# Optimization experiments

Measured on AMD Instinct MI355X. Metric: run time of the kernel, lower is better.

Reference implementation:

```python
import jax, jax.numpy as jnp
import numpy as np

B, S, D = 2, 2048, 2048
H, KVH, DH = 16, 4, 128  # n_heads, n_kv_heads, head_dim
N_REP = H // KVH
THETA = 10000.0


def setup_inputs() -> dict:
    key = jax.random.key(0)
    ks = jax.random.split(key, 6)
    x = jax.random.normal(ks[0], (B, S, D), dtype=jnp.float32)
    wq = jax.random.normal(ks[1], (H * DH, D), dtype=jnp.float32) * (D ** -0.5)
    wk = jax.random.normal(ks[2], (KVH * DH, D), dtype=jnp.float32) * (D ** -0.5)
    wv = jax.random.normal(ks[3], (KVH * DH, D), dtype=jnp.float32) * (D ** -0.5)
    wo = jax.random.normal(ks[4], (D, H * DH), dtype=jnp.float32) * (D ** -0.5)
    # RoPE frequencies (complex freqs -> cos/sin), shape [S, DH//2]
    inv_freq = 1.0 / (THETA ** (np.arange(0, DH, 2, dtype=np.float32) / DH))
    angles = np.arange(S, dtype=np.float32)[:, None] * inv_freq[None, :]
    freqs_cos = jnp.asarray(np.cos(angles))
    freqs_sin = jnp.asarray(np.sin(angles))
    # causal additive mask [1,1,S,S]
    neg = jnp.full((S, S), -1e9, dtype=jnp.float32)
    mask = jnp.triu(neg, k=1)[None, None]
    return {"x": x, "freqs_cos": freqs_cos, "freqs_sin": freqs_sin,
            "mask": mask, "wq": wq, "wk": wk, "wv": wv, "wo": wo}


def _rope(t, cos, sin):
    # t: [B,S,h,DH]; cos/sin: [S,DH//2] -> broadcast [1,S,1,DH//2]
    tp = t.reshape(*t.shape[:-1], -1, 2)
    tr, ti = tp[..., 0], tp[..., 1]
    c = cos[None, :, None, :]
    s = sin[None, :, None, :]
    out_r = tr * c - ti * s
    out_i = tr * s + ti * c
    return jnp.stack([out_r, out_i], axis=-1).reshape(t.shape)


def reference(x, freqs_cos, freqs_sin, mask, wq, wk, wv, wo):
    b, s, _ = x.shape
    xq = jnp.einsum('bsd,ed->bse', x, wq).reshape(b, s, H, DH)
    xk = jnp.einsum('bsd,ed->bse', x, wk).reshape(b, s, KVH, DH)
    xv = jnp.einsum('bsd,ed->bse', x, wv).reshape(b, s, KVH, DH)
    xq = _rope(xq, freqs_cos, freqs_sin)
    xk = _rope(xk, freqs_cos, freqs_sin)
    # GQA: repeat kv heads
    xk = jnp.repeat(xk, N_REP, axis=2)
    xv = jnp.repeat(xv, N_REP, axis=2)
    q = xq.transpose(0, 2, 1, 3)  # [B,H,S,DH]
    k = xk.transpose(0, 2, 1, 3)
    v = xv.transpose(0, 2, 1, 3)
    scores = jnp.einsum('bhqd,bhkd->bhqk', q, k) / jnp.sqrt(jnp.float32(DH))
    scores = scores + mask
    attn = jax.nn.softmax(scores.astype(jnp.float32), axis=-1).astype(q.dtype)
    out = jnp.einsum('bhqk,bhkd->bhqd', attn, v)
    out = out.transpose(0, 2, 1, 3).reshape(b, s, H * DH)
    return jnp.einsum('bse,de->bsd', out, wo)
```

## Files before the change

kernel.cpp:

```cpp
#include <hip/hip_runtime.h>

#define Bq   2
#define Sq   2048
#define Dq   2048
#define Hq   16
#define KVHq 4
#define DHq  128

typedef unsigned short u16;
typedef short  bf16x8 __attribute__((ext_vector_type(8)));
typedef float  f32x4  __attribute__((ext_vector_type(4)));
typedef float  f32x16 __attribute__((ext_vector_type(16)));
typedef unsigned short u16x2 __attribute__((ext_vector_type(2)));
typedef unsigned short u16x4 __attribute__((ext_vector_type(4)));
typedef unsigned uu32x4 __attribute__((ext_vector_type(4)));

__device__ __forceinline__ u16 f2bf(float f) {
    unsigned u = __float_as_uint(f);
    u += 0x7fffu + ((u >> 16) & 1u);
    return (u16)(u >> 16);
}
__device__ __forceinline__ float bf2f(u16 s) {
    return __uint_as_float(((unsigned)s) << 16);
}

__device__ __forceinline__ unsigned cvtpk(float a, float b) {
    unsigned r;
    asm("v_cvt_pk_bf16_f32 %0, %1, %2" : "=v"(r) : "v"(a), "v"(b));
    return r;
}
__device__ __forceinline__ void pl32swap(unsigned& a, unsigned& b) {
    asm("v_permlane32_swap_b32 %0, %1" : "+v"(a), "+v"(b));
}
__device__ __forceinline__ bf16x8 mkfrag(unsigned w0, unsigned w1, unsigned w2, unsigned w3) {
    uu32x4 t = {w0, w1, w2, w3};
    return __builtin_bit_cast(bf16x8, t);
}

__global__ void cast_all(const float* __restrict__ x,
                         const float* __restrict__ wq, const float* __restrict__ wk,
                         const float* __restrict__ wv, const float* __restrict__ wo,
                         u16* __restrict__ xb, u16* __restrict__ wqb,
                         u16* __restrict__ wkvb, u16* __restrict__ wob) {
    int i = blockIdx.x * 256 + threadIdx.x;
    const float4* src; u16x4* dst; int off;
    if (i < 2097152) { src = (const float4*)x; dst = (u16x4*)xb; off = i; }
    else {
        int j = i - 2097152;
        if (j < 1048576)      { src = (const float4*)wq; dst = (u16x4*)wqb;  off = j; }
        else if (j < 1310720) { src = (const float4*)wk; dst = (u16x4*)wkvb; off = j - 1048576; }
        else if (j < 1572864) { src = (const float4*)wv; dst = (u16x4*)wkvb + 262144; off = j - 1310720; }
        else                  { src = (const float4*)wo; dst = (u16x4*)wob;  off = j - 1572864; }
    }
    float4 v = src[off];
    u16x4 o;
    o.x = f2bf(v.x); o.y = f2bf(v.y); o.z = f2bf(v.z); o.w = f2bf(v.w);
    dst[off] = o;
}

__device__ __forceinline__ void async16(const void* g, void* l) {
    __builtin_amdgcn_global_load_lds(
        (const __attribute__((address_space(1))) unsigned*)g,
        (__attribute__((address_space(3))) unsigned*)l, 16, 0, 0);
}

__device__ __forceinline__ void stc(u16* p, float v)   { *p = f2bf(v); }
__device__ __forceinline__ void stc(float* p, float v) { *p = v; }

template <typename OutT>
__global__ __launch_bounds__(256) void gemm_nt(
    const u16* __restrict__ A, const u16* __restrict__ W, OutT* __restrict__ C,
    int M, int N, int K)
{
    __shared__ __align__(16) u16 lA0[128 * 32], lA1[128 * 32];
    __shared__ __align__(16) u16 lB0[128 * 32], lB1[128 * 32];

    const int t    = threadIdx.x;
    const int w    = t >> 6;
    const int lane = t & 63;
    const int lr   = lane & 15;
    const int quad = lane >> 4;
    const int wm   = (w >> 1) * 64, wn = (w & 1) * 64;
    const int bm   = blockIdx.x * 128, bn = blockIdx.y * 128;

    const u16* Ab = A + (size_t)bm * K;
    const u16* Wb = W + (size_t)bn * K;

    const int r0  = t >> 2;
    const int r1  = 64 + (t >> 2);
    const int kc0 = (t & 3) * 8;

    f32x4 acc[4][4] = {};

    auto STAGE = [&](int kt, u16* la, u16* lb) {
        async16(Ab + (size_t)r0 * K + kt + kc0, (char*)la + w * 1024);
        async16(Ab + (size_t)r1 * K + kt + kc0, (char*)la + 4096 + w * 1024);
        async16(Wb + (size_t)r0 * K + kt + kc0, (char*)lb + w * 1024);
        async16(Wb + (size_t)r1 * K + kt + kc0, (char*)lb + 4096 + w * 1024);
    };
    auto COMPUTE = [&](const u16* la, const u16* lb) {
        bf16x8 af[4], bfr[4];
#pragma unroll
        for (int i = 0; i < 4; i++)
            af[i] = *(const bf16x8*)&la[(wm + i * 16 + lr) * 32 + quad * 8];
#pragma unroll
        for (int j = 0; j < 4; j++)
            bfr[j] = *(const bf16x8*)&lb[(wn + j * 16 + lr) * 32 + quad * 8];
#pragma unroll
        for (int i = 0; i < 4; i++)
#pragma unroll
            for (int j = 0; j < 4; j++)
                acc[i][j] = __builtin_amdgcn_mfma_f32_16x16x32_bf16(af[i], bfr[j], acc[i][j], 0, 0, 0);
    };

    STAGE(0, lA0, lB0);
    __syncthreads();

    for (int kt = 0; kt < K; kt += 64) {
        if (kt + 32 < K) STAGE(kt + 32, lA1, lB1);
        COMPUTE(lA0, lB0);
        __syncthreads();
        if (kt + 64 < K) STAGE(kt + 64, lA0, lB0);
        COMPUTE(lA1, lB1);
        __syncthreads();
    }

#pragma unroll
    for (int i = 0; i < 4; i++)
#pragma unroll
        for (int j = 0; j < 4; j++)
#pragma unroll
            for (int r = 0; r < 4; r++) {
                int gm = bm + wm + i * 16 + quad * 4 + r;
                int gn = bn + wn + j * 16 + lr;
                stc(C + (size_t)gm * N + gn, acc[i][j][r]);
            }
}

__global__ __launch_bounds__(256) void gemm_qkv(
    const u16* __restrict__ A, const u16* __restrict__ W,
    u16* __restrict__ Qo, u16* __restrict__ KVo,
    const float* __restrict__ Cs, const float* __restrict__ Sn)
{
    __shared__ __align__(16) u16 lA0[128 * 32], lA1[128 * 32];
    __shared__ __align__(16) u16 lB0[128 * 32], lB1[128 * 32];
    const int K = 2048;

    const int t    = threadIdx.x;
    const int w    = t >> 6;
    const int lane = t & 63;
    const int lr   = lane & 15;
    const int quad = lane >> 4;
    const int wm   = (w >> 1) * 64, wn = (w & 1) * 64;
    const int bm   = blockIdx.x * 128, bn = blockIdx.y * 128;

    const u16* Ab = A + (size_t)bm * K;
    const u16* Wb = W + (size_t)bn * K;

    const int r0  = t >> 2;
    const int r1  = 64 + (t >> 2);
    const int kc0 = (t & 3) * 8;

    f32x4 acc[4][4] = {};

    auto STAGE = [&](int kt, u16* la, u16* lb) {
        async16(Ab + (size_t)r0 * K + kt + kc0, (char*)la + w * 1024);
        async16(Ab + (size_t)r1 * K + kt + kc0, (char*)la + 4096 + w * 1024);
        async16(Wb + (size_t)r0 * K + kt + kc0, (char*)lb + w * 1024);
        async16(Wb + (size_t)r1 * K + kt + kc0, (char*)lb + 4096 + w * 1024);
    };
    auto COMPUTE = [&](const u16* la, const u16* lb) {
        bf16x8 af[4], bfr[4];
#pragma unroll
        for (int i = 0; i < 4; i++)
            af[i] = *(const bf16x8*)&la[(wm + i * 16 + lr) * 32 + quad * 8];
#pragma unroll
        for (int j = 0; j < 4; j++)
            bfr[j] = *(const bf16x8*)&lb[(wn + j * 16 + lr) * 32 + quad * 8];
#pragma unroll
        for (int i = 0; i < 4; i++)
#pragma unroll
            for (int j = 0; j < 4; j++)
                acc[i][j] = __builtin_amdgcn_mfma_f32_16x16x32_bf16(af[i], bfr[j], acc[i][j], 0, 0, 0);
    };

    STAGE(0, lA0, lB0);
    __syncthreads();

    for (int kt = 0; kt < K; kt += 64) {
        if (kt + 32 < K) STAGE(kt + 32, lA1, lB1);
        COMPUTE(lA0, lB0);
        __syncthreads();
        if (kt + 64 < K) STAGE(kt + 64, lA0, lB0);
        COMPUTE(lA1, lB1);
        __syncthreads();
    }

    const bool doRope = (bn < 2560);
    const bool isQ    = (bn < 2048);
#pragma unroll
    for (int i = 0; i < 4; i++)
#pragma unroll
        for (int j = 0; j < 4; j++)
#pragma unroll
            for (int r = 0; r < 4; r++) {
                const int gm = bm + wm + i * 16 + quad * 4 + r;
                const int gn = bn + wn + j * 16 + lr;
                float v  = acc[i][j][r];
                float pv = __shfl_xor(v, 1);
                if (doRope) {
                    const int s = gm & (Sq - 1);
                    const int p = (gn & 127) >> 1;
                    const float cc = Cs[s * 64 + p], ss = Sn[s * 64 + p];
                    v = (gn & 1) ? (pv * ss + v * cc) : (v * cc - pv * ss);
                }
                const u16 ov = f2bf(v);
                if (isQ) Qo [(size_t)gm * 2048 + gn]          = ov;
                else     KVo[(size_t)gm * 1024 + (gn - 2048)] = ov;
            }
}

__global__ void transpose_v_k(const u16* __restrict__ KV, u16* __restrict__ Vt) {
    __shared__ u16 tile[32][33];
    const int bk = blockIdx.z;
    const int b = bk >> 2, kvh = bk & 3;
    const int s0 = blockIdx.x * 32, d0 = blockIdx.y * 32;
    const int tx = threadIdx.x, ty = threadIdx.y;
    tile[ty][tx] = KV[(size_t)(b * Sq + s0 + ty) * 1024 + 512 + kvh * 128 + d0 + tx];
    __syncthreads();
    Vt[((size_t)bk * DHq + d0 + ty) * Sq + s0 + tx] = tile[tx][ty];
}

#define PSCALE 0.12753102f
#define PBIAS  17.31234049f

__global__ __launch_bounds__(256, 2) void flash_attn_sk2(
    const u16* __restrict__ Q, const u16* __restrict__ KV,
    const u16* __restrict__ Vt, u16* __restrict__ Oc, float* __restrict__ Lc)
{
    __shared__ __align__(16) u16 kl[2][4 * 64 * 32];
    __shared__ __align__(16) u16 vl[2][2 * 128 * 32];

    const int did = (int)blockIdx.y * 32 + (int)blockIdx.x;
    const int nf  = (did & 7) * 160 + (did >> 3);
    const int bh  = nf / 40;
    const int c   = 39 - (nf % 40);

    const int b = bh >> 4, h = bh & 15;
    const int kvh = h >> 2;
    int qt, ci, nc;
    if (c < 4)       { qt = c;                    ci = 0;            nc = 1; }
    else if (c < 12) { qt = 4  + ((c - 4) >> 1);  ci = (c - 4) & 1;  nc = 2; }
    else if (c < 24) { qt = 8  + (c - 12) / 3;    ci = (c - 12) % 3; nc = 3; }
    else             { qt = 12 + ((c - 24) >> 2); ci = (c - 24) & 3; nc = 4; }
    const int T  = 2 * (qt + 1);
    const int t0 = (ci * T) / nc, t1 = ((ci + 1) * T) / nc;

    const int tid = threadIdx.x;
    const int w = tid >> 6, lane = tid & 63;
    const int col = lane & 31, hi = lane >> 5;
    const int q0 = qt * 128 + w * 32;
    const int qg = q0 + col;

    const u16* Qp = Q + (size_t)(b * Sq + qg) * (Hq * DHq) + h * DHq + hi * 8;
    bf16x8 qf[8];
#pragma unroll
    for (int ks = 0; ks < 8; ks++) qf[ks] = *(const bf16x8*)(Qp + ks * 16);

    const u16* Kg = KV + (size_t)b * Sq * 1024 + kvh * DHq;
    const u16* Vg = Vt + (size_t)(b * KVHq + kvh) * DHq * Sq;

    const int srow = lane >> 2;
    const int swl  = ((lane & 3) ^ ((lane >> 3) & 3)) * 8;
    const int xsw  = (col >> 1) & 3;

    f32x16 o[4] = {};
    float lsum = 0.f;

    auto STAGE = [&](int kt, int bsel) {
        const int kb = kt * 64;
#pragma unroll
        for (int c4 = 0; c4 < 4; c4++) {
            const u16* g = Kg + (size_t)(kb + w * 16 + srow) * 1024 + c4 * 32 + swl;
            async16(g, (char*)kl[bsel] + (c4 * 2048 + w * 512) * 2 + lane * 16);
        }
#pragma unroll
        for (int c4 = 0; c4 < 4; c4++) {
            const int g2 = c4 & 1, dbase = (c4 >> 1) * 64;
            const u16* g = Vg + (size_t)(dbase + w * 16 + srow) * Sq + kb + g2 * 32 + swl;
            async16(g, (char*)vl[bsel] + (g2 * 4096 + (dbase + w * 16) * 32) * 2 + lane * 16);
        }
    };

    STAGE(t0, 0);
    __syncthreads();

    int cur = 0;
    for (int kt = t0; kt < t1; kt++) {
        if (kt + 1 < t1) STAGE(kt + 1, cur ^ 1);

        const int kb = kt * 64;
        const u16* klc = kl[cur];
        const u16* vlc = vl[cur];

        f32x16 s0 = {}, s1 = {};
        __builtin_amdgcn_s_setprio(1);
#pragma unroll
        for (int ks = 0; ks < 8; ks++) {
            const int ch     = (((ks & 1) * 2 + hi) ^ xsw) * 8;
            const int kkbase = (ks >> 1) * 2048 + ch;
            bf16x8 k0 = *(const bf16x8*)&klc[kkbase + col * 32];
            bf16x8 k1 = *(const bf16x8*)&klc[kkbase + (32 + col) * 32];
            s0 = __builtin_amdgcn_mfma_f32_32x32x16_bf16(k0, qf[ks], s0, 0, 0, 0);
            s1 = __builtin_amdgcn_mfma_f32_32x32x16_bf16(k1, qf[ks], s1, 0, 0, 0);
        }
        __builtin_amdgcn_s_setprio(0);

        float p0a[16], p1a[16];
        float ls = 0.f;
        if (q0 - kb >= 63) {
#pragma unroll
            for (int r = 0; r < 16; r++) {
                float a0 = exp2f(s0[r] * PSCALE - PBIAS);
                float a1 = exp2f(s1[r] * PSCALE - PBIAS);
                ls += a0 + a1;
                p0a[r] = a0; p1a[r] = a1;
            }
        } else {
            const int thr = qg - kb;
#pragma unroll
            for (int r = 0; r < 16; r++) {
                const int kloc = (r & 3) + 8 * (r >> 2) + 4 * hi;
                float a0 = (kloc <= thr)      ? exp2f(s0[r] * PSCALE - PBIAS) : 0.f;
                float a1 = (kloc + 32 <= thr) ? exp2f(s1[r] * PSCALE - PBIAS) : 0.f;
                ls += a0 + a1;
                p0a[r] = a0; p1a[r] = a1;
            }
        }
        lsum += ls;

        __builtin_amdgcn_s_setprio(1);
#define PV_HALF(PARR, KSBASE)                                                      \
        {                                                                          \
            _Pragma("unroll")                                                      \
            for (int k2 = 0; k2 < 2; k2++) {                                       \
                const int bb = k2 * 8;                                             \
                unsigned wa = cvtpk(PARR[bb + 0], PARR[bb + 1]);                   \
                unsigned wb = cvtpk(PARR[bb + 4], PARR[bb + 5]);                   \
                pl32swap(wa, wb);                                                  \
                unsigned wc = cvtpk(PARR[bb + 2], PARR[bb + 3]);                   \
                unsigned wd = cvtpk(PARR[bb + 6], PARR[bb + 7]);                   \
                pl32swap(wc, wd);                                                  \
                bf16x8 pa = mkfrag(wa, wc, wb, wd);                                \
                const int vch   = ((k2 * 2 + hi) ^ xsw) * 8;                       \
                const int vbase = (((KSBASE) >> 1) * 4096) + vch;                  \
                _Pragma("unroll")                                                  \
                for (int n = 0; n < 4; n++) {                                      \
                    bf16x8 vf = *(const bf16x8*)&vlc[vbase + (n * 32 + col) * 32]; \
                    o[n] = __builtin_amdgcn_mfma_f32_32x32x16_bf16(pa, vf, o[n], 0, 0, 0); \
                }                                                                  \
            }                                                                      \
        }
        PV_HALF(p0a, 0)
        PV_HALF(p1a, 2)
#undef PV_HALF
        __builtin_amdgcn_s_setprio(0);

        if (kt + 1 < t1) __syncthreads();
        cur ^= 1;
    }

    float tot = lsum + __shfl_xor(lsum, 32);
    u16*   Ocb = Oc + (size_t)(bh * 40 + c) * 16384 + (size_t)w * 32 * 128;
    float* Lcb = Lc + (size_t)(bh * 40 + c) * 128 + w * 32;
    if (hi == 0) Lcb[col] = tot;
#pragma unroll
    for (int r = 0; r < 16; r++) {
        const int rloc = (r & 3) + 8 * (r >> 2) + 4 * hi;
#pragma unroll
        for (int n = 0; n < 4; n++)
            Ocb[rloc * 128 + n * 32 + col] = f2bf(o[n][r]);
    }
}

__global__ __launch_bounds__(256) void flash_reduce2(
    const u16* __restrict__ Oc, const float* __restrict__ Lc, u16* __restrict__ AO)
{
    const int bh = blockIdx.x;
    const int qt = blockIdx.y;
    const int e  = blockIdx.z * 256 + threadIdx.x;
    const int row = e >> 5, col4 = e & 31;
    int cst, nc;
    if (qt < 4)       { cst = qt;                 nc = 1; }
    else if (qt < 8)  { cst = 4  + 2 * (qt - 4);  nc = 2; }
    else if (qt < 12) { cst = 12 + 3 * (qt - 8);  nc = 3; }
    else              { cst = 24 + 4 * (qt - 12); nc = 4; }
    float a0 = 0.f, a1 = 0.f, a2 = 0.f, a3 = 0.f;
    float l = 0.f;
    for (int i = 0; i < nc; i++) {
        const size_t base = (size_t)(bh * 40 + cst + i);
        const u16x4 vv = ((const u16x4*)(Oc + base * 16384))[e];
        a0 += bf2f(vv.x); a1 += bf2f(vv.y); a2 += bf2f(vv.z); a3 += bf2f(vv.w);
        l  += Lc[base * 128 + row];
    }
    const float inv = 1.0f / l;
    const int b = bh >> 4, h = bh & 15;
    u16x4 ov;
    ov.x = f2bf(a0 * inv); ov.y = f2bf(a1 * inv);
    ov.z = f2bf(a2 * inv); ov.w = f2bf(a3 * inv);
    u16* dst = AO + (size_t)(b * Sq + qt * 128 + row) * (Hq * DHq) + h * DHq + col4 * 4;
    *(u16x4*)dst = ov;
}

__global__ __launch_bounds__(256) void flash_attn(
    const u16* __restrict__ Q, const u16* __restrict__ KV,
    const u16* __restrict__ Vt, u16* __restrict__ O)
{
    __shared__ __align__(16) u16 plds[4][16 * 72];
    const int bh = blockIdx.x;
    const int b = bh >> 4, h = bh & 15;
    const int kvh = h >> 2;
    const int w = threadIdx.x >> 6, lane = threadIdx.x & 63;
    const int lr = lane & 15, quad = lane >> 4;
    const int yy = gridDim.y - 1 - blockIdx.y;
    const int q0 = yy * 64 + w * 16;

    const u16* Qp = Q + (size_t)(b * Sq + q0 + lr) * (Hq * DHq) + h * DHq + quad * 8;
    bf16x8 qf[4];
#pragma unroll
    for (int kk = 0; kk < 4; kk++) qf[kk] = *(const bf16x8*)(Qp + kk * 32);

    const u16* Kp = KV + (size_t)b * Sq * 1024 + kvh * DHq;
    const u16* Vp = Vt + (size_t)(b * KVHq + kvh) * DHq * Sq;

    f32x4 o[8] = {};
    float lsum[4] = {0.f, 0.f, 0.f, 0.f};

    const int nt = (q0 + 16 + 63) >> 6;
    for (int kt = 0; kt < nt; kt++) {
        const int kb = kt * 64;
        f32x4 s[4] = {};
#pragma unroll
        for (int kk = 0; kk < 4; kk++) {
#pragma unroll
            for (int j = 0; j < 4; j++) {
                bf16x8 kf = *(const bf16x8*)(Kp + (size_t)(kb + j * 16 + lr) * 1024 + kk * 32 + quad * 8);
                s[j] = __builtin_amdgcn_mfma_f32_16x16x32_bf16(qf[kk], kf, s[j], 0, 0, 0);
            }
        }
#pragma unroll
        for (int r = 0; r < 4; r++) {
            const int qg = q0 + quad * 4 + r;
#pragma unroll
            for (int j = 0; j < 4; j++) {
                float v = s[j][r] * PSCALE - PBIAS;
                float p = (kb + j * 16 + lr <= qg) ? exp2f(v) : 0.f;
                lsum[r] += p;
                plds[w][(quad * 4 + r) * 72 + j * 16 + lr] = f2bf(p);
            }
        }
        bf16x8 pa0 = *(const bf16x8*)&plds[w][lr * 72 + quad * 8];
        bf16x8 pa1 = *(const bf16x8*)&plds[w][lr * 72 + 32 + quad * 8];
#pragma unroll
        for (int dt = 0; dt < 8; dt++) {
            bf16x8 v0 = *(const bf16x8*)(Vp + (size_t)(dt * 16 + lr) * Sq + kb + quad * 8);
            bf16x8 v1 = *(const bf16x8*)(Vp + (size_t)(dt * 16 + lr) * Sq + kb + 32 + quad * 8);
            o[dt] = __builtin_amdgcn_mfma_f32_16x16x32_bf16(pa0, v0, o[dt], 0, 0, 0);
            o[dt] = __builtin_amdgcn_mfma_f32_16x16x32_bf16(pa1, v1, o[dt], 0, 0, 0);
        }
    }

    u16* Ob = O + (size_t)(b * Sq) * (Hq * DHq) + h * DHq;
#pragma unroll
    for (int r = 0; r < 4; r++) {
        float t = lsum[r];
        t += __shfl_xor(t, 1);
        t += __shfl_xor(t, 2);
        t += __shfl_xor(t, 4);
        t += __shfl_xor(t, 8);
        const float inv = 1.0f / t;
        const int qg = q0 + quad * 4 + r;
#pragma unroll
        for (int dt = 0; dt < 8; dt++)
            Ob[(size_t)qg * (Hq * DHq) + dt * 16 + lr] = f2bf(o[dt][r] * inv);
    }
}

extern "C" void kernel_launch(void* const* d_in, const int* in_sizes, int n_in,
                              void* d_out, int out_size, void* d_ws, size_t ws_size,
                              hipStream_t stream) {
    const float* x  = (const float*)d_in[0];
    const float* fc = (const float*)d_in[1];
    const float* fs = (const float*)d_in[2];
    const float* wq = (const float*)d_in[4];
    const float* wk = (const float*)d_in[5];
    const float* wv = (const float*)d_in[6];
    const float* wo = (const float*)d_in[7];
    float* out = (float*)d_out;

    char* ws = (char*)d_ws;
    u16* xb   = (u16*)(ws);
    u16* wqb  = (u16*)(ws + 16777216);
    u16* wkvb = (u16*)(ws + 25165824);
    u16* wob  = (u16*)(ws + 29360128);
    u16* Qb   = (u16*)(ws + 37748736);
    u16* KVb  = (u16*)(ws + 54525952);
    u16* Vtb  = (u16*)(ws + 62914560);
    u16* AOb  = (u16*)(ws + 67108864);
    u16* Ocb  = (u16*)(ws + 83886080);
    float* Lcb = (float*)(ws + 167772160);
    const size_t WS_NEED = 168427520;

    cast_all<<<18432, 256, 0, stream>>>(x, wq, wk, wv, wo, xb, wqb, wkvb, wob);

    dim3 blk(256);
    gemm_qkv<<<dim3(32, 24), blk, 0, stream>>>(xb, wqb, Qb, KVb, fc, fs);

    transpose_v_k<<<dim3(64, 4, 8), dim3(32, 32), 0, stream>>>(KVb, Vtb);

    if (ws_size >= WS_NEED) {
        flash_attn_sk2<<<dim3(32, 40), blk, 0, stream>>>(Qb, KVb, Vtb, Ocb, Lcb);
        flash_reduce2<<<dim3(32, 16, 16), blk, 0, stream>>>(Ocb, Lcb, AOb);
    } else {
        flash_attn<<<dim3(32, 32), blk, 0, stream>>>(Qb, KVb, Vtb, AOb);
    }

    gemm_nt<float><<<dim3(32, 16), blk, 0, stream>>>(AOb, wob, out, 4096, 2048, 2048);
}
```

Measured before the change: 347.3 us.

## Fuse x fp32-to-bf16 cast into QKV GEMM A-tile loading

Removes the separate cast of the 4096x2048 activation x to bf16. The QKV GEMM now stages fp32 x tiles directly into LDS with an XOR swizzle and converts them to bf16 fragments with v_cvt_pk_bf16_f32 at compute time. This saves one full write and re-read of x through global memory. In exchange the GEMM moves twice the A bytes into LDS, uses twice the A-tile LDS space, and adds conversion instructions to the inner loop. That load is repeated for each of the 24 column blocks.

```diff
diff --git a/kernel.cpp b/kernel.cpp
--- a/kernel.cpp
+++ b/kernel.cpp
@@ -37,21 +37,16 @@
     return __builtin_bit_cast(bf16x8, t);
 }
 
-__global__ void cast_all(const float* __restrict__ x,
-                         const float* __restrict__ wq, const float* __restrict__ wk,
+__global__ void cast_all(const float* __restrict__ wq, const float* __restrict__ wk,
                          const float* __restrict__ wv, const float* __restrict__ wo,
-                         u16* __restrict__ xb, u16* __restrict__ wqb,
-                         u16* __restrict__ wkvb, u16* __restrict__ wob) {
-    int i = blockIdx.x * 256 + threadIdx.x;
+                         u16* __restrict__ wqb, u16* __restrict__ wkvb,
+                         u16* __restrict__ wob) {
+    int j = blockIdx.x * 256 + threadIdx.x;
     const float4* src; u16x4* dst; int off;
-    if (i < 2097152) { src = (const float4*)x; dst = (u16x4*)xb; off = i; }
-    else {
-        int j = i - 2097152;
-        if (j < 1048576)      { src = (const float4*)wq; dst = (u16x4*)wqb;  off = j; }
-        else if (j < 1310720) { src = (const float4*)wk; dst = (u16x4*)wkvb; off = j - 1048576; }
-        else if (j < 1572864) { src = (const float4*)wv; dst = (u16x4*)wkvb + 262144; off = j - 1310720; }
-        else                  { src = (const float4*)wo; dst = (u16x4*)wob;  off = j - 1572864; }
-    }
+    if (j < 1048576)      { src = (const float4*)wq; dst = (u16x4*)wqb;  off = j; }
+    else if (j < 1310720) { src = (const float4*)wk; dst = (u16x4*)wkvb; off = j - 1048576; }
+    else if (j < 1572864) { src = (const float4*)wv; dst = (u16x4*)wkvb + 262144; off = j - 1310720; }
+    else                  { src = (const float4*)wo; dst = (u16x4*)wob;  off = j - 1572864; }
     float4 v = src[off];
     u16x4 o;
     o.x = f2bf(v.x); o.y = f2bf(v.y); o.z = f2bf(v.z); o.w = f2bf(v.w);
@@ -138,12 +133,12 @@
 }
 
 __global__ __launch_bounds__(256) void gemm_qkv(
-    const u16* __restrict__ A, const u16* __restrict__ W,
+    const float* __restrict__ X, const u16* __restrict__ W,
     u16* __restrict__ Qo, u16* __restrict__ KVo,
     const float* __restrict__ Cs, const float* __restrict__ Sn)
 {
-    __shared__ __align__(16) u16 lA0[128 * 32], lA1[128 * 32];
-    __shared__ __align__(16) u16 lB0[128 * 32], lB1[128 * 32];
+    __shared__ __align__(16) float lA0[128 * 32], lA1[128 * 32];
+    __shared__ __align__(16) u16   lB0[128 * 32], lB1[128 * 32];
     const int K = 2048;
 
     const int t    = threadIdx.x;
@@ -154,26 +149,38 @@
     const int wm   = (w >> 1) * 64, wn = (w & 1) * 64;
     const int bm   = blockIdx.x * 128, bn = blockIdx.y * 128;
 
-    const u16* Ab = A + (size_t)bm * K;
-    const u16* Wb = W + (size_t)bn * K;
+    const float* Ax = X + (size_t)bm * K;
+    const u16*   Wb = W + (size_t)bn * K;
 
     const int r0  = t >> 2;
     const int r1  = 64 + (t >> 2);
     const int kc0 = (t & 3) * 8;
+    const int rsub = lane >> 3;
+    const int asw  = ((lane & 7) ^ (lane >> 3)) * 4;
+    const int p0b  = ((2 * quad) ^ (lr & 7)) * 16;
+    const int p1b  = ((2 * quad + 1) ^ (lr & 7)) * 16;
 
     f32x4 acc[4][4] = {};
 
-    auto STAGE = [&](int kt, u16* la, u16* lb) {
-        async16(Ab + (size_t)r0 * K + kt + kc0, (char*)la + w * 1024);
-        async16(Ab + (size_t)r1 * K + kt + kc0, (char*)la + 4096 + w * 1024);
+    auto STAGE = [&](int kt, float* la, u16* lb) {
+#pragma unroll
+        for (int l = 0; l < 4; l++) {
+            const int row = (l * 4 + w) * 8 + rsub;
+            async16(Ax + (size_t)row * K + kt + asw, (char*)la + (l * 4 + w) * 1024);
+        }
         async16(Wb + (size_t)r0 * K + kt + kc0, (char*)lb + w * 1024);
         async16(Wb + (size_t)r1 * K + kt + kc0, (char*)lb + 4096 + w * 1024);
     };
-    auto COMPUTE = [&](const u16* la, const u16* lb) {
+    auto COMPUTE = [&](const float* la, const u16* lb) {
         bf16x8 af[4], bfr[4];
 #pragma unroll
-        for (int i = 0; i < 4; i++)
-            af[i] = *(const bf16x8*)&la[(wm + i * 16 + lr) * 32 + quad * 8];
+        for (int i = 0; i < 4; i++) {
+            const int rb = (wm + i * 16 + lr) * 128;
+            f32x4 lo = *(const f32x4*)((const char*)la + rb + p0b);
+            f32x4 hi = *(const f32x4*)((const char*)la + rb + p1b);
+            af[i] = mkfrag(cvtpk(lo.x, lo.y), cvtpk(lo.z, lo.w),
+                           cvtpk(hi.x, hi.y), cvtpk(hi.z, hi.w));
+        }
 #pragma unroll
         for (int j = 0; j < 4; j++)
             bfr[j] = *(const bf16x8*)&lb[(wn + j * 16 + lr) * 32 + quad * 8];
@@ -499,7 +506,6 @@
     float* out = (float*)d_out;
 
     char* ws = (char*)d_ws;
-    u16* xb   = (u16*)(ws);
     u16* wqb  = (u16*)(ws + 16777216);
     u16* wkvb = (u16*)(ws + 25165824);
     u16* wob  = (u16*)(ws + 29360128);
@@ -511,10 +517,10 @@
     float* Lcb = (float*)(ws + 167772160);
     const size_t WS_NEED = 168427520;
 
-    cast_all<<<18432, 256, 0, stream>>>(x, wq, wk, wv, wo, xb, wqb, wkvb, wob);
+    cast_all<<<10240, 256, 0, stream>>>(wq, wk, wv, wo, wqb, wkvb, wob);
 
     dim3 blk(256);
-    gemm_qkv<<<dim3(32, 24), blk, 0, stream>>>(xb, wqb, Qb, KVb, fc, fs);
+    gemm_qkv<<<dim3(32, 24), blk, 0, stream>>>(x, wqb, Qb, KVb, fc, fs);
 
     transpose_v_k<<<dim3(64, 4, 8), dim3(32, 32), 0, stream>>>(KVb, Vtb);
 
```

After: 368.2 us. +6.0%, slower.
